# Kernel optimization log

Hardware: AMD Instinct MI355X
Metric: run time of the kernel (lower is better)

## Reference

```python
import jax, jax.numpy as jnp
import numpy as np
import math

LOG_2PI = math.log(2.0 * math.pi)


def setup_inputs() -> dict:
    key = jax.random.key(0)
    k_x, k_mu = jax.random.split(key, 2)
    B, T, S, M, D = 8, 4096, 64, 8, 128
    return {
        "X": jax.random.normal(k_x, (B, T, D), dtype=jnp.float32),
        "pi_logits": jnp.zeros((S,), dtype=jnp.float32),
        "trans_logits": jnp.zeros((S, S), dtype=jnp.float32),
        "weight_logits": jnp.zeros((S, M), dtype=jnp.float32),
        "means": jax.random.normal(k_mu, (S, M, D), dtype=jnp.float32),
        "log_vars": jnp.zeros((S, M, D), dtype=jnp.float32),
    }


def reference(X, pi_logits, trans_logits, weight_logits, means, log_vars):
    # X: [B,T,D]; means/log_vars: [S,M,D]
    D = X.shape[-1]
    inv_vars = jnp.exp(-log_vars)                                   # [S,M,D]
    # -0.5 * sum_d (x_d - mu_d)^2 / var_d, expanded as GEMMs (same math):
    a = jnp.einsum('btd,smd->btsm', X * X, inv_vars)                # sum x^2/var
    b = jnp.einsum('btd,smd->btsm', X, means * inv_vars)            # sum x*mu/var
    c = jnp.sum(means * means * inv_vars, axis=-1)                  # [S,M]
    exp_term = -0.5 * (a - 2.0 * b + c[None, None, :, :])           # [B,T,S,M]
    log_norm = -0.5 * (jnp.sum(log_vars, axis=-1) + D * LOG_2PI)    # [S,M]
    log_mix_w = jax.nn.log_softmax(weight_logits, axis=1)           # [S,M]
    # emission log-prob per state: logsumexp over mixture components
    emis = jax.scipy.special.logsumexp(
        exp_term + (log_norm + log_mix_w)[None, None], axis=-1)     # [B,T,S]

    log_pi = jax.nn.log_softmax(pi_logits)                          # [S]
    log_A = jax.nn.log_softmax(trans_logits, axis=1)                # [S,S]

    alpha0 = log_pi[None, :] + emis[:, 0]                           # [B,S]
    emis_t = jnp.swapaxes(emis, 0, 1)                               # [T,B,S]

    def step(alpha, e_t):
        # alpha: [B,S]; log-semiring matvec: logsumexp_i(alpha_i + A_ij)
        nxt = e_t + jax.scipy.special.logsumexp(
            alpha[:, :, None] + log_A[None, :, :], axis=1)
        return nxt, None

    alpha_T, _ = jax.lax.scan(step, alpha0, emis_t[1:])
    return jax.scipy.special.logsumexp(alpha_T, axis=-1)            # [B]
```

## Files before the change

kernel.cpp:

```cpp
#include <hip/hip_runtime.h>
#include <hip/hip_bf16.h>
#include <math.h>

#define LOG2PI_F 1.8378770664093453f
#define EPAD 68

typedef __attribute__((ext_vector_type(8))) short bf16x8;
typedef __attribute__((ext_vector_type(4))) float f32x4;
typedef __attribute__((ext_vector_type(16))) float f32x16;

static __device__ inline short f2bf(float x) {
  __hip_bfloat16 h = __float2bfloat16(x);
  return *reinterpret_cast<short*>(&h);
}
static __device__ inline unsigned cvtpk(float lo, float hi) {
  unsigned r;
  asm("v_cvt_pk_bf16_f32 %0, %1, %2" : "=v"(r) : "v"(lo), "v"(hi));
  return r;
}
static __device__ inline f32x4 mfma16(bf16x8 a, bf16x8 b, f32x4 c) {
  return __builtin_amdgcn_mfma_f32_16x16x32_bf16(a, b, c, 0, 0, 0);
}
static __device__ inline f32x16 mfma32(bf16x8 a, bf16x8 b, f32x16 c) {
  return __builtin_amdgcn_mfma_f32_32x32x16_bf16(a, b, c, 0, 0, 0);
}

__global__ __launch_bounds__(256) void mmm_prep_fused(
    const float* __restrict__ tl, const float* __restrict__ means,
    const float* __restrict__ log_vars, const float* __restrict__ weight_logits,
    const float* __restrict__ X,
    short* __restrict__ WTbf, short* __restrict__ Gt,
    float* __restrict__ const_c, short* __restrict__ XeP) {
  __shared__ float red[4];
  int bid = blockIdx.x;
  int tid = threadIdx.x;

  if (bid < 64) {
    if (tid < 64) {
      int r = bid, lane = tid;
      float v = tl[r * 64 + lane];
      float mx = v;
      #pragma unroll
      for (int off = 1; off < 64; off <<= 1) mx = fmaxf(mx, __shfl_xor(mx, off));
      float e = expf(v - mx);
      float s = e;
      #pragma unroll
      for (int off = 1; off < 64; off <<= 1) s += __shfl_xor(s, off);
      WTbf[lane * 64 + r] = f2bf(e / s);
    }
    return;
  }

  if (bid < 320) {
    int h = tid >> 7, d = tid & 127;
    int sm = (bid - 64) * 2 + h;
    int s = sm >> 3, m = sm & 7;
    float lv = log_vars[sm * 128 + d];
    float iv = expf(-lv);
    float mu = means[sm * 128 + d];
    float miv = mu * iv;
    Gt[sm * 256 + d] = f2bf(miv);
    Gt[sm * 256 + 128 + d] = f2bf(-0.5f * iv);
    float v = mu * miv + lv;
    #pragma unroll
    for (int off = 1; off < 64; off <<= 1) v += __shfl_xor(v, off);
    if ((tid & 63) == 0) red[tid >> 6] = v;
    __syncthreads();
    if (d == 0) {
      float tot = red[2 * h] + red[2 * h + 1];
      float wl[8];
      float mx = -3.4e38f;
      #pragma unroll
      for (int j = 0; j < 8; ++j) { wl[j] = weight_logits[s * 8 + j]; mx = fmaxf(mx, wl[j]); }
      float sum = 0.f;
      #pragma unroll
      for (int j = 0; j < 8; ++j) sum += expf(wl[j] - mx);
      float lmw = wl[m] - mx - logf(sum);
      const_c[sm] = -0.5f * (tot + 128.0f * LOG2PI_F) + lmw;
    }
    return;
  }

  int kbid = bid - 320;
  int q = kbid >> 7;
  int bt = ((kbid & 127) << 8) + tid;
  const float4* src = (const float4*)(X + (size_t)bt * 128 + q * 32);
  float xv[32];
  #pragma unroll
  for (int i = 0; i < 8; ++i) {
    float4 v = src[i];
    xv[4 * i] = v.x; xv[4 * i + 1] = v.y; xv[4 * i + 2] = v.z; xv[4 * i + 3] = v.w;
  }
  size_t base1 = ((size_t)q * 32768 + bt) * 32;
  size_t base2 = ((size_t)(q + 4) * 32768 + bt) * 32;
  int bx = bt & 3;
  #pragma unroll
  for (int g = 0; g < 4; ++g) {
    unsigned w1[4], w2[4];
    #pragma unroll
    for (int j = 0; j < 4; ++j) {
      float a = xv[g * 8 + 2 * j], c = xv[g * 8 + 2 * j + 1];
      w1[j] = cvtpk(a, c);
      w2[j] = cvtpk(a * a, c * c);
    }
    int gs = (g ^ bx) * 8;
    *(uint4*)&XeP[base1 + gs] = *(uint4*)w1;
    *(uint4*)&XeP[base2 + gs] = *(uint4*)w2;
  }
}

__global__ __launch_bounds__(512) void mmm_emischunk_kernel(
    const short* __restrict__ Gt, const short* __restrict__ XeP,
    const float* __restrict__ const_c, const short* __restrict__ WTbf,
    short* __restrict__ NTb, float* __restrict__ aux,
    float* __restrict__ ehat0, float* __restrict__ cmax0) {
  __shared__ __align__(16) short Bt[16384];
  __shared__ __align__(16) float ccs[512];
  __shared__ float wavemax[8][64];
  __shared__ float colmax2[2][64];
  __shared__ __align__(16) float elds[2][64 * EPAD];
  int tid = threadIdx.x;
  int w = tid >> 6, lane = tid & 63, lr = lane & 15, lg = lane >> 4;
  int T0 = (blockIdx.x & 63) * 64;

  ccs[tid] = const_c[tid];

  bf16x8 gf[4][8];
  #pragma unroll
  for (int rt = 0; rt < 4; ++rt) {
    int row = w * 64 + rt * 16 + lr;
    #pragma unroll
    for (int kc = 0; kc < 8; ++kc)
      gf[rt][kc] = *(const bf16x8*)&Gt[row * 256 + kc * 32 + lg * 8];
  }

  uint4 sreg[4];
  {
    size_t bt0 = (size_t)blockIdx.x * 64;
    #pragma unroll
    for (int r = 0; r < 4; ++r) {
      int ofs = r * 8192 + tid * 16;
      int kb2 = ofs >> 12, rem = ofs & 4095;
      sreg[r] = *(const uint4*)((const char*)XeP + ((size_t)kb2 * 32768 + bt0) * 64 + rem);
    }
  }

  for (int it = 0; it < 2; ++it) {
    int bcur = (blockIdx.x + it * 256) >> 6;
    __syncthreads();
    #pragma unroll
    for (int r = 0; r < 4; ++r)
      *(uint4*)((char*)Bt + r * 8192 + tid * 16) = sreg[r];
    __syncthreads();
    if (it == 0) {
      size_t bt0n = ((size_t)blockIdx.x + 256) * 64;
      #pragma unroll
      for (int r = 0; r < 4; ++r) {
        int ofs = r * 8192 + tid * 16;
        int kb2 = ofs >> 12, rem = ofs & 4095;
        sreg[r] = *(const uint4*)((const char*)XeP + ((size_t)kb2 * 32768 + bt0n) * 64 + rem);
      }
    }

    f32x4 acc[4][4];
    #pragma unroll
    for (int rt = 0; rt < 4; ++rt)
      #pragma unroll
      for (int ct = 0; ct < 4; ++ct)
        acc[rt][ct] = (f32x4){0.f, 0.f, 0.f, 0.f};

    #pragma unroll
    for (int kc = 0; kc < 8; ++kc) {
      bf16x8 bfr[4];
      #pragma unroll
      for (int ct = 0; ct < 4; ++ct) {
        int btL = ct * 16 + lr;
        bfr[ct] = *(const bf16x8*)&Bt[kc * 2048 + btL * 32 + ((lg ^ (btL & 3)) * 8)];
      }
      #pragma unroll
      for (int rt = 0; rt < 4; ++rt)
        #pragma unroll
        for (int ct = 0; ct < 4; ++ct)
          acc[rt][ct] = mfma16(gf[rt][kc], bfr[ct], acc[rt][ct]);
    }

    float lse[4][4];
    #pragma unroll
    for (int rt = 0; rt < 4; ++rt) {
      f32x4 cc = *(f32x4*)&ccs[w * 64 + rt * 16 + lg * 4];
      #pragma unroll
      for (int ct = 0; ct < 4; ++ct) {
        f32x4 v = acc[rt][ct] + cc;
        float mx = fmaxf(fmaxf(v[0], v[1]), fmaxf(v[2], v[3]));
        mx = fmaxf(mx, __shfl_xor(mx, 16));
        float sum = expf(v[0] - mx) + expf(v[1] - mx) + expf(v[2] - mx) + expf(v[3] - mx);
        sum += __shfl_xor(sum, 16);
        lse[rt][ct] = mx + logf(sum);
      }
    }
    #pragma unroll
    for (int ct = 0; ct < 4; ++ct) {
      float cm = fmaxf(fmaxf(lse[0][ct], lse[1][ct]), fmaxf(lse[2][ct], lse[3][ct]));
      cm = fmaxf(cm, __shfl_xor(cm, 32));
      if (lg == 0) wavemax[w][ct * 16 + lr] = cm;
    }
    __syncthreads();
    if (w == 0) {
      float cm = wavemax[0][lane];
      #pragma unroll
      for (int ww = 1; ww < 8; ++ww) cm = fmaxf(cm, wavemax[ww][lane]);
      colmax2[it][lane] = cm;
      if (lane == 0 && T0 == 0) cmax0[bcur] = cm;
    }
    __syncthreads();
    #pragma unroll
    for (int ct = 0; ct < 4; ++ct) {
      float cm = colmax2[it][ct * 16 + lr];
      #pragma unroll
      for (int rt = 0; rt < 4; ++rt) {
        float v = expf(lse[rt][ct] - cm);
        if (!(lg & 1)) {
          int s = w * 8 + rt * 2 + (lg >> 1);
          elds[it][(ct * 16 + lr) * EPAD + s] = v;
          if (T0 == 0 && ct == 0 && lr == 0) ehat0[bcur * 64 + s] = v;
        }
      }
    }
  }
  __syncthreads();

  int tl = w >> 2, q = w & 3;
  int bS = (blockIdx.x + tl * 256) >> 6;
  int c = (T0 >> 4) + q;
  int t0l, nsteps;
  if (c == 0) { t0l = 1; nsteps = 15; } else { t0l = q * 16; nsteps = 16; }
  int l31 = lane & 31, hi = lane >> 5;
  const float* etile = &elds[tl][0];

  bf16x8 af[2][4];
  #pragma unroll
  for (int wi = 0; wi < 2; ++wi)
    #pragma unroll
    for (int kb = 0; kb < 4; ++kb)
      af[wi][kb] = *(const bf16x8*)&WTbf[(wi * 32 + l31) * 64 + kb * 16 + hi * 8];

  unsigned P[2][2][4][2];
  #pragma unroll
  for (int s = 0; s < 2; ++s) {
    int col = s * 32 + l31;
    #pragma unroll
    for (int cm = 0; cm < 2; ++cm)
      #pragma unroll
      for (int qq = 0; qq < 4; ++qq)
        #pragma unroll
        for (int p = 0; p < 2; ++p) {
          int row = 32 * cm + 8 * qq + 4 * hi + 2 * p;
          unsigned lo = (row == col) ? 0x3F80u : 0u;
          unsigned h16 = (row + 1 == col) ? 0x3F80u : 0u;
          P[s][cm][qq][p] = lo | (h16 << 16);
        }
  }

  float logscale = 0.f;
  f32x4 ecur[2][4], enxt[2][4];
  #pragma unroll
  for (int cm = 0; cm < 2; ++cm)
    #pragma unroll
    for (int qq = 0; qq < 4; ++qq)
      ecur[cm][qq] = *(const f32x4*)&etile[t0l * EPAD + cm * 32 + qq * 8 + hi * 4];

  for (int i = 0; i < nsteps; ++i) {
    if (i + 1 < nsteps) {
      #pragma unroll
      for (int cm = 0; cm < 2; ++cm)
        #pragma unroll
        for (int qq = 0; qq < 4; ++qq)
          enxt[cm][qq] = *(const f32x4*)&etile[(t0l + i + 1) * EPAD + cm * 32 + qq * 8 + hi * 4];
    }

    __builtin_amdgcn_s_setprio(1);
    #pragma unroll
    for (int s = 0; s < 2; ++s) {
      bf16x8 B[4];
      #pragma unroll
      for (int kb = 0; kb < 4; ++kb) {
        int cm = kb >> 1, kbl = kb & 1;
        int4 wrd;
        #pragma unroll
        for (int p = 0; p < 2; ++p) {
          unsigned avv = P[s][cm][2 * kbl + 1][p];
          unsigned bvv = P[s][cm][2 * kbl][p];
          asm("v_permlane32_swap_b32 %0, %1" : "+v"(avv), "+v"(bvv));
          if (p == 0) { wrd.x = (int)bvv; wrd.z = (int)avv; }
          else        { wrd.y = (int)bvv; wrd.w = (int)avv; }
        }
        B[kb] = *(bf16x8*)&wrd;
      }

      f32x16 d0, d1;
      #pragma unroll
      for (int r = 0; r < 16; ++r) { d0[r] = 0.f; d1[r] = 0.f; }
      #pragma unroll
      for (int kb = 0; kb < 4; ++kb) {
        d0 = mfma32(af[0][kb], B[kb], d0);
        d1 = mfma32(af[1][kb], B[kb], d1);
      }

      #pragma unroll
      for (int qq = 0; qq < 4; ++qq)
        #pragma unroll
        for (int p = 0; p < 2; ++p) {
          P[s][0][qq][p] = cvtpk(d0[4 * qq + 2 * p] * ecur[0][qq][2 * p],
                                 d0[4 * qq + 2 * p + 1] * ecur[0][qq][2 * p + 1]);
          P[s][1][qq][p] = cvtpk(d1[4 * qq + 2 * p] * ecur[1][qq][2 * p],
                                 d1[4 * qq + 2 * p + 1] * ecur[1][qq][2 * p + 1]);
        }
    }
    __builtin_amdgcn_s_setprio(0);

    if ((i & 7) == 7) {
      float m = 0.f;
      #pragma unroll
      for (int s = 0; s < 2; ++s)
        #pragma unroll
        for (int cm = 0; cm < 2; ++cm)
          #pragma unroll
          for (int qq = 0; qq < 4; ++qq)
            #pragma unroll
            for (int p = 0; p < 2; ++p) {
              unsigned u = P[s][cm][qq][p];
              m = fmaxf(m, __uint_as_float(u << 16));
              m = fmaxf(m, __uint_as_float(u & 0xffff0000u));
            }
      #pragma unroll
      for (int off = 1; off < 64; off <<= 1) m = fmaxf(m, __shfl_xor(m, off));
      float inv = 1.0f / m;
      #pragma unroll
      for (int s = 0; s < 2; ++s)
        #pragma unroll
        for (int cm = 0; cm < 2; ++cm)
          #pragma unroll
          for (int qq = 0; qq < 4; ++qq)
            #pragma unroll
            for (int p = 0; p < 2; ++p) {
              unsigned u = P[s][cm][qq][p];
              P[s][cm][qq][p] = cvtpk(__uint_as_float(u << 16) * inv,
                                      __uint_as_float(u & 0xffff0000u) * inv);
            }
      logscale += logf(m);
    }

    #pragma unroll
    for (int cm = 0; cm < 2; ++cm)
      #pragma unroll
      for (int qq = 0; qq < 4; ++qq) ecur[cm][qq] = enxt[cm][qq];
  }

  unsigned short* No = (unsigned short*)(NTb + (((size_t)bS * 256 + c) << 12));
  #pragma unroll
  for (int s = 0; s < 2; ++s)
    #pragma unroll
    for (int cm = 0; cm < 2; ++cm)
      #pragma unroll
      for (int qq = 0; qq < 4; ++qq)
        #pragma unroll
        for (int p = 0; p < 2; ++p) {
          int row = 32 * cm + 8 * qq + 4 * hi + 2 * p;
          int col = s * 32 + l31;
          unsigned u = P[s][cm][qq][p];
          No[row * 64 + col] = (unsigned short)(u & 0xffffu);
          No[(row + 1) * 64 + col] = (unsigned short)(u >> 16);
        }

  float cs = (lane < nsteps) ? colmax2[tl][t0l + lane] : 0.f;
  #pragma unroll
  for (int off = 1; off < 64; off <<= 1) cs += __shfl_xor(cs, off);
  if (lane == 0) aux[(size_t)bS * 256 + c] = cs + logscale;
}

__global__ __launch_bounds__(256) void mmm_merge_kernel(
    const short* __restrict__ NTb, const float* __restrict__ aux,
    float* __restrict__ G2T, float* __restrict__ auxg) {
  int g = blockIdx.x, b = blockIdx.y;
  int tid = threadIdx.x;
  int w = tid >> 6, lane = tid & 63;
  int wi = w >> 1, wj = w & 1;
  int lr = lane & 15, lg = lane >> 4;

  __shared__ __align__(16) short L[2][4096];
  __shared__ float wmax[4];

  for (int idx = tid; idx < 4096; idx += 256) {
    int j = idx >> 6, k = idx & 63;
    L[0][idx ^ ((j & 7) << 3)] = (j == k) ? (short)0x3F80 : (short)0;
  }
  __syncthreads();

  int cbase = b * 256 + g * 8;

  float logscale = 0.f;
  int cur = 0;
  f32x4 acc[2][2];

  bf16x8 apre[2][2];
  {
    const short* Mc = NTb + ((size_t)cbase << 12);
    #pragma unroll
    for (int rt = 0; rt < 2; ++rt)
      #pragma unroll
      for (int kc = 0; kc < 2; ++kc)
        apre[rt][kc] = *(const bf16x8*)&Mc[(wi * 32 + rt * 16 + lr) * 64 + kc * 32 + lg * 8];
  }

  for (int cc = 0; cc < 8; ++cc) {
    bf16x8 acur[2][2];
    #pragma unroll
    for (int rt = 0; rt < 2; ++rt)
      #pragma unroll
      for (int kc = 0; kc < 2; ++kc) acur[rt][kc] = apre[rt][kc];
    if (cc < 7) {
      const short* Mc = NTb + ((size_t)(cbase + cc + 1) << 12);
      #pragma unroll
      for (int rt = 0; rt < 2; ++rt)
        #pragma unroll
        for (int kc = 0; kc < 2; ++kc)
          apre[rt][kc] = *(const bf16x8*)&Mc[(wi * 32 + rt * 16 + lr) * 64 + kc * 32 + lg * 8];
    }

    logscale += aux[cbase + cc];

    bf16x8 bfr[2][2];
    #pragma unroll
    for (int ct = 0; ct < 2; ++ct) {
      int j = wj * 32 + ct * 16 + lr;
      int sw = (j & 7) << 3;
      #pragma unroll
      for (int kc = 0; kc < 2; ++kc)
        bfr[ct][kc] = *(const bf16x8*)&L[cur][(j * 64 + kc * 32 + lg * 8) ^ sw];
    }

    #pragma unroll
    for (int rt = 0; rt < 2; ++rt)
      #pragma unroll
      for (int ct = 0; ct < 2; ++ct) {
        f32x4 c = {0.f, 0.f, 0.f, 0.f};
        c = mfma16(acur[rt][0], bfr[ct][0], c);
        c = mfma16(acur[rt][1], bfr[ct][1], c);
        acc[rt][ct] = c;
      }

    if ((cc & 3) == 3) {
      float m = 0.f;
      #pragma unroll
      for (int rt = 0; rt < 2; ++rt)
        #pragma unroll
        for (int ct = 0; ct < 2; ++ct)
          #pragma unroll
          for (int r = 0; r < 4; ++r) m = fmaxf(m, acc[rt][ct][r]);
      #pragma unroll
      for (int off = 1; off < 64; off <<= 1) m = fmaxf(m, __shfl_xor(m, off));
      if (lane == 0) wmax[w] = m;
      __syncthreads();
      m = fmaxf(fmaxf(wmax[0], wmax[1]), fmaxf(wmax[2], wmax[3]));
      float inv = 1.0f / m;
      #pragma unroll
      for (int rt = 0; rt < 2; ++rt)
        #pragma unroll
        for (int ct = 0; ct < 2; ++ct) acc[rt][ct] *= inv;
      logscale += logf(m);
    }

    int nxt = cur ^ 1;
    unsigned* L32 = (unsigned*)&L[nxt][0];
    #pragma unroll
    for (int rt = 0; rt < 2; ++rt)
      #pragma unroll
      for (int ct = 0; ct < 2; ++ct) {
        int row0 = wi * 32 + rt * 16 + lg * 4;
        int col = wj * 32 + ct * 16 + lr;
        int sidx = (col * 64 + row0) ^ ((col & 7) << 3);
        L32[(sidx >> 1) + 0] = cvtpk(acc[rt][ct][0], acc[rt][ct][1]);
        L32[(sidx >> 1) + 1] = cvtpk(acc[rt][ct][2], acc[rt][ct][3]);
      }
    __syncthreads();
    cur = nxt;
  }

  float* Mo = G2T + (((size_t)b * 32 + g) << 12);
  #pragma unroll
  for (int rt = 0; rt < 2; ++rt)
    #pragma unroll
    for (int ct = 0; ct < 2; ++ct)
      #pragma unroll
      for (int r = 0; r < 4; ++r) {
        int row = wi * 32 + rt * 16 + lg * 4 + r;
        int col = wj * 32 + ct * 16 + lr;
        Mo[row * 64 + col] = acc[rt][ct][r];
      }

  if (w == 0 && lane == 0) auxg[b * 32 + g] = logscale;
}

__global__ __launch_bounds__(64) void mmm_combine_kernel(
    const float* __restrict__ pi_logits, const float* __restrict__ ehat0,
    const float* __restrict__ cmax0, const float* __restrict__ G2T,
    const float* __restrict__ auxg, float* __restrict__ out) {
  int b = blockIdx.x, lane = threadIdx.x;
  __shared__ __align__(16) float alds[64];

  float pv = pi_logits[lane];
  float mx = pv;
  #pragma unroll
  for (int off = 1; off < 64; off <<= 1) mx = fmaxf(mx, __shfl_xor(mx, off));
  float pe = expf(pv - mx);
  float ps = pe;
  #pragma unroll
  for (int off = 1; off < 64; off <<= 1) ps += __shfl_xor(ps, off);

  float a = (pe / ps) * ehat0[b * 64 + lane];
  double logtot = (double)cmax0[b];
  alds[lane] = a;
  __builtin_amdgcn_wave_barrier();

  const float* Mb = G2T + (((size_t)b * 32) << 12) + lane * 64;
  f32x4 mc[16], mn[16];
  #pragma unroll
  for (int i = 0; i < 16; ++i) mc[i] = *(const f32x4*)&Mb[i * 4];

  for (int g = 0; g < 32; ++g) {
    if (g < 31) {
      const float* Mn = Mb + ((size_t)(g + 1) << 12);
      #pragma unroll
      for (int i = 0; i < 16; ++i) mn[i] = *(const f32x4*)&Mn[i * 4];
    }
    f32x4 a4 = {0.f, 0.f, 0.f, 0.f};
    #pragma unroll
    for (int i = 0; i < 16; ++i) {
      f32x4 av = *(const f32x4*)&alds[i * 4];
      a4 += mc[i] * av;
    }
    float acc = (a4[0] + a4[1]) + (a4[2] + a4[3]);
    float s = acc;
    #pragma unroll
    for (int off = 1; off < 64; off <<= 1) s += __shfl_xor(s, off);
    logtot += (double)(auxg[b * 32 + g] + logf(s));
    float an = acc / s;
    __builtin_amdgcn_wave_barrier();
    alds[lane] = an;
    __builtin_amdgcn_wave_barrier();
    #pragma unroll
    for (int i = 0; i < 16; ++i) mc[i] = mn[i];
  }
  if (lane == 0) out[b] = (float)logtot;
}

extern "C" void kernel_launch(void* const* d_in, const int* in_sizes, int n_in,
                              void* d_out, int out_size, void* d_ws, size_t ws_size,
                              hipStream_t stream) {
  const float* X      = (const float*)d_in[0];
  const float* pi_l   = (const float*)d_in[1];
  const float* tr_l   = (const float*)d_in[2];
  const float* wl     = (const float*)d_in[3];
  const float* means  = (const float*)d_in[4];
  const float* lvs    = (const float*)d_in[5];
  float* out = (float*)d_out;

  float* ws = (float*)d_ws;
  short* Gt      = (short*)ws;
  float* const_c = ws + 65536;
  short* WTbf    = (short*)(ws + 66048);
  float* ehat0   = ws + 68096;
  float* cmax0   = ws + 68608;
  short* XeP     = (short*)(ws + 2198528);
  short* NTb     = (short*)(ws + 6392832);
  float* aux     = ws + 10587136;
  float* G2T     = ws + 10591232;
  float* auxg    = ws + 11639808;

  mmm_prep_fused<<<832, 256, 0, stream>>>(tr_l, means, lvs, wl, X,
                                          WTbf, Gt, const_c, XeP);
  mmm_emischunk_kernel<<<256, 512, 0, stream>>>(Gt, XeP, const_c, WTbf,
                                                NTb, aux, ehat0, cmax0);
  mmm_merge_kernel<<<dim3(32, 8), 256, 0, stream>>>(NTb, aux, G2T, auxg);
  mmm_combine_kernel<<<8, 64, 0, stream>>>(pi_l, ehat0, cmax0, G2T, auxg, out);
}
```

Before: 100.5 us.

## Split emission-chunk kernel to one time tile per block, doubling grid

```diff
diff --git a/kernel.cpp b/kernel.cpp
--- a/kernel.cpp
+++ b/kernel.cpp
@@ -114,14 +114,17 @@
     const float* __restrict__ const_c, const short* __restrict__ WTbf,
     short* __restrict__ NTb, float* __restrict__ aux,
     float* __restrict__ ehat0, float* __restrict__ cmax0) {
-  __shared__ __align__(16) short Bt[16384];
+  __shared__ __align__(16) char ubuf[32768];
   __shared__ __align__(16) float ccs[512];
   __shared__ float wavemax[8][64];
-  __shared__ float colmax2[2][64];
-  __shared__ __align__(16) float elds[2][64 * EPAD];
+  __shared__ float colmax[64];
+  short* Bt = (short*)ubuf;
+  float* elds = (float*)ubuf;
   int tid = threadIdx.x;
   int w = tid >> 6, lane = tid & 63, lr = lane & 15, lg = lane >> 4;
-  int T0 = (blockIdx.x & 63) * 64;
+  int bid = blockIdx.x;
+  int b = bid >> 6;
+  int T0 = (bid & 63) * 64;
 
   ccs[tid] = const_c[tid];
 
@@ -136,7 +139,7 @@
 
   uint4 sreg[4];
   {
-    size_t bt0 = (size_t)blockIdx.x * 64;
+    size_t bt0 = (size_t)bid * 64;
     #pragma unroll
     for (int r = 0; r < 4; ++r) {
       int ofs = r * 8192 + tid * 16;
@@ -145,97 +148,83 @@
     }
   }
 
-  for (int it = 0; it < 2; ++it) {
-    int bcur = (blockIdx.x + it * 256) >> 6;
-    __syncthreads();
-    #pragma unroll
-    for (int r = 0; r < 4; ++r)
-      *(uint4*)((char*)Bt + r * 8192 + tid * 16) = sreg[r];
-    __syncthreads();
-    if (it == 0) {
-      size_t bt0n = ((size_t)blockIdx.x + 256) * 64;
-      #pragma unroll
-      for (int r = 0; r < 4; ++r) {
-        int ofs = r * 8192 + tid * 16;
-        int kb2 = ofs >> 12, rem = ofs & 4095;
-        sreg[r] = *(const uint4*)((const char*)XeP + ((size_t)kb2 * 32768 + bt0n) * 64 + rem);
+  #pragma unroll
+  for (int r = 0; r < 4; ++r)
+    *(uint4*)((char*)Bt + r * 8192 + tid * 16) = sreg[r];
+  __syncthreads();
+
+  f32x4 acc[4][4];
+  #pragma unroll
+  for (int rt = 0; rt < 4; ++rt)
+    #pragma unroll
+    for (int ct = 0; ct < 4; ++ct)
+      acc[rt][ct] = (f32x4){0.f, 0.f, 0.f, 0.f};
+
+  #pragma unroll
+  for (int kc = 0; kc < 8; ++kc) {
+    bf16x8 bfr[4];
+    #pragma unroll
+    for (int ct = 0; ct < 4; ++ct) {
+      int btL = ct * 16 + lr;
+      bfr[ct] = *(const bf16x8*)&Bt[kc * 2048 + btL * 32 + ((lg ^ (btL & 3)) * 8)];
+    }
+    #pragma unroll
+    for (int rt = 0; rt < 4; ++rt)
+      #pragma unroll
+      for (int ct = 0; ct < 4; ++ct)
+        acc[rt][ct] = mfma16(gf[rt][kc], bfr[ct], acc[rt][ct]);
+  }
+
+  float lse[4][4];
+  #pragma unroll
+  for (int rt = 0; rt < 4; ++rt) {
+    f32x4 cc = *(f32x4*)&ccs[w * 64 + rt * 16 + lg * 4];
+    #pragma unroll
+    for (int ct = 0; ct < 4; ++ct) {
+      f32x4 v = acc[rt][ct] + cc;
+      float mx = fmaxf(fmaxf(v[0], v[1]), fmaxf(v[2], v[3]));
+      mx = fmaxf(mx, __shfl_xor(mx, 16));
+      float sum = expf(v[0] - mx) + expf(v[1] - mx) + expf(v[2] - mx) + expf(v[3] - mx);
+      sum += __shfl_xor(sum, 16);
+      lse[rt][ct] = mx + logf(sum);
+    }
+  }
+  #pragma unroll
+  for (int ct = 0; ct < 4; ++ct) {
+    float cm = fmaxf(fmaxf(lse[0][ct], lse[1][ct]), fmaxf(lse[2][ct], lse[3][ct]));
+    cm = fmaxf(cm, __shfl_xor(cm, 32));
+    if (lg == 0) wavemax[w][ct * 16 + lr] = cm;
+  }
+  __syncthreads();
+  if (w == 0) {
+    float cm = wavemax[0][lane];
+    #pragma unroll
+    for (int ww = 1; ww < 8; ++ww) cm = fmaxf(cm, wavemax[ww][lane]);
+    colmax[lane] = cm;
+    if (lane == 0 && T0 == 0) cmax0[b] = cm;
+  }
+  __syncthreads();
+  #pragma unroll
+  for (int ct = 0; ct < 4; ++ct) {
+    float cm = colmax[ct * 16 + lr];
+    #pragma unroll
+    for (int rt = 0; rt < 4; ++rt) {
+      float v = expf(lse[rt][ct] - cm);
+      if (!(lg & 1)) {
+        int s = w * 8 + rt * 2 + (lg >> 1);
+        elds[(ct * 16 + lr) * EPAD + s] = v;
+        if (T0 == 0 && ct == 0 && lr == 0) ehat0[b * 64 + s] = v;
       }
     }
-
-    f32x4 acc[4][4];
-    #pragma unroll
-    for (int rt = 0; rt < 4; ++rt)
-      #pragma unroll
-      for (int ct = 0; ct < 4; ++ct)
-        acc[rt][ct] = (f32x4){0.f, 0.f, 0.f, 0.f};
-
-    #pragma unroll
-    for (int kc = 0; kc < 8; ++kc) {
-      bf16x8 bfr[4];
-      #pragma unroll
-      for (int ct = 0; ct < 4; ++ct) {
-        int btL = ct * 16 + lr;
-        bfr[ct] = *(const bf16x8*)&Bt[kc * 2048 + btL * 32 + ((lg ^ (btL & 3)) * 8)];
-      }
-      #pragma unroll
-      for (int rt = 0; rt < 4; ++rt)
-        #pragma unroll
-        for (int ct = 0; ct < 4; ++ct)
-          acc[rt][ct] = mfma16(gf[rt][kc], bfr[ct], acc[rt][ct]);
-    }
-
-    float lse[4][4];
-    #pragma unroll
-    for (int rt = 0; rt < 4; ++rt) {
-      f32x4 cc = *(f32x4*)&ccs[w * 64 + rt * 16 + lg * 4];
-      #pragma unroll
-      for (int ct = 0; ct < 4; ++ct) {
-        f32x4 v = acc[rt][ct] + cc;
-        float mx = fmaxf(fmaxf(v[0], v[1]), fmaxf(v[2], v[3]));
-        mx = fmaxf(mx, __shfl_xor(mx, 16));
-        float sum = expf(v[0] - mx) + expf(v[1] - mx) + expf(v[2] - mx) + expf(v[3] - mx);
-        sum += __shfl_xor(sum, 16);
-        lse[rt][ct] = mx + logf(sum);
-      }
-    }
-    #pragma unroll
-    for (int ct = 0; ct < 4; ++ct) {
-      float cm = fmaxf(fmaxf(lse[0][ct], lse[1][ct]), fmaxf(lse[2][ct], lse[3][ct]));
-      cm = fmaxf(cm, __shfl_xor(cm, 32));
-      if (lg == 0) wavemax[w][ct * 16 + lr] = cm;
-    }
-    __syncthreads();
-    if (w == 0) {
-      float cm = wavemax[0][lane];
-      #pragma unroll
-      for (int ww = 1; ww < 8; ++ww) cm = fmaxf(cm, wavemax[ww][lane]);
-      colmax2[it][lane] = cm;
-      if (lane == 0 && T0 == 0) cmax0[bcur] = cm;
-    }
-    __syncthreads();
-    #pragma unroll
-    for (int ct = 0; ct < 4; ++ct) {
-      float cm = colmax2[it][ct * 16 + lr];
-      #pragma unroll
-      for (int rt = 0; rt < 4; ++rt) {
-        float v = expf(lse[rt][ct] - cm);
-        if (!(lg & 1)) {
-          int s = w * 8 + rt * 2 + (lg >> 1);
-          elds[it][(ct * 16 + lr) * EPAD + s] = v;
-          if (T0 == 0 && ct == 0 && lr == 0) ehat0[bcur * 64 + s] = v;
-        }
-      }
-    }
   }
   __syncthreads();
 
-  int tl = w >> 2, q = w & 3;
-  int bS = (blockIdx.x + tl * 256) >> 6;
+  if (w >= 4) return;
+  int q = w;
   int c = (T0 >> 4) + q;
   int t0l, nsteps;
   if (c == 0) { t0l = 1; nsteps = 15; } else { t0l = q * 16; nsteps = 16; }
   int l31 = lane & 31, hi = lane >> 5;
-  const float* etile = &elds[tl][0];
 
   bf16x8 af[2][4];
   #pragma unroll
@@ -267,7 +256,7 @@
   for (int cm = 0; cm < 2; ++cm)
     #pragma unroll
     for (int qq = 0; qq < 4; ++qq)
-      ecur[cm][qq] = *(const f32x4*)&etile[t0l * EPAD + cm * 32 + qq * 8 + hi * 4];
+      ecur[cm][qq] = *(const f32x4*)&elds[t0l * EPAD + cm * 32 + qq * 8 + hi * 4];
 
   for (int i = 0; i < nsteps; ++i) {
     if (i + 1 < nsteps) {
@@ -275,7 +264,7 @@
       for (int cm = 0; cm < 2; ++cm)
         #pragma unroll
         for (int qq = 0; qq < 4; ++qq)
-          enxt[cm][qq] = *(const f32x4*)&etile[(t0l + i + 1) * EPAD + cm * 32 + qq * 8 + hi * 4];
+          enxt[cm][qq] = *(const f32x4*)&elds[(t0l + i + 1) * EPAD + cm * 32 + qq * 8 + hi * 4];
     }
 
     __builtin_amdgcn_s_setprio(1);
@@ -356,7 +345,7 @@
       for (int qq = 0; qq < 4; ++qq) ecur[cm][qq] = enxt[cm][qq];
   }
 
-  unsigned short* No = (unsigned short*)(NTb + (((size_t)bS * 256 + c) << 12));
+  unsigned short* No = (unsigned short*)(NTb + (((size_t)b * 256 + c) << 12));
   #pragma unroll
   for (int s = 0; s < 2; ++s)
     #pragma unroll
@@ -372,10 +361,10 @@
           No[(row + 1) * 64 + col] = (unsigned short)(u >> 16);
         }
 
-  float cs = (lane < nsteps) ? colmax2[tl][t0l + lane] : 0.f;
+  float cs = (lane < nsteps) ? colmax[t0l + lane] : 0.f;
   #pragma unroll
   for (int off = 1; off < 64; off <<= 1) cs += __shfl_xor(cs, off);
-  if (lane == 0) aux[(size_t)bS * 256 + c] = cs + logscale;
+  if (lane == 0) aux[(size_t)b * 256 + c] = cs + logscale;
 }
 
 __global__ __launch_bounds__(256) void mmm_merge_kernel(
@@ -579,7 +568,7 @@
 
   mmm_prep_fused<<<832, 256, 0, stream>>>(tr_l, means, lvs, wl, X,
                                           WTbf, Gt, const_c, XeP);
-  mmm_emischunk_kernel<<<256, 512, 0, stream>>>(Gt, XeP, const_c, WTbf,
+  mmm_emischunk_kernel<<<512, 512, 0, stream>>>(Gt, XeP, const_c, WTbf,
                                                 NTb, aux, ehat0, cmax0);
   mmm_merge_kernel<<<dim3(32, 8), 256, 0, stream>>>(NTb, aux, G2T, auxg);
   mmm_combine_kernel<<<8, 64, 0, stream>>>(pi_l, ehat0, cmax0, G2T, auxg, out);
```

After: 110.0 us. 1.09x slower.
